# Kernel optimization log

Measured on AMD Instinct MI355X. Metric: run time of the kernel, lower is better.

The kernel has to match this reference:

```python
import jax, jax.numpy as jnp
import numpy as np

H, W, C = 64, 64, 2048
IMG = 224


def setup_inputs() -> dict:
    key = jax.random.key(0)
    features = jax.random.normal(key, (2, H, W, C), dtype=jnp.float32)
    return {"features": features, "img_size": IMG}


def reference(features, img_size):
    # features: [2, H, W, C] -- query (index 0) and target (index 1) feature maps.
    x0 = features[0]  # [H, W, C]
    x1 = features[1]  # [H, W, C]
    # Correlation volume: Decomposition[i,j,k,l] = sum_c x0[i,j,c] * x1[k,l,c]
    # (replaces the quadruple Python loop with a single GEMM-shaped einsum)
    decom = jnp.einsum('ijc,klc->ijkl', x0, x1)  # [H, W, H, W]
    decom = decom / jnp.max(decom)
    # NOTE: source calls `Decomposition.clamp(min=0)` without assignment -> no-op.
    decom_1 = jnp.sum(decom, axis=(2, 3))  # [H, W] saliency on query image
    decom_2 = jnp.sum(decom, axis=(0, 1))  # [H, W] saliency on target image
    stacked = jnp.stack((decom_1, decom_2))  # [2, H, W]
    # F.interpolate(mode='bilinear', align_corners=False) == half-pixel bilinear resize
    out = jax.image.resize(stacked, (2, img_size, img_size), method='bilinear')
    return out  # [2, img_size, img_size]
```

## Files before the change

kernel.cpp:

```cpp
#include <hip/hip_runtime.h>
#include <hip/hip_bf16.h>

#define HW    4096
#define CDIM  2048
#define IMG   224
#define NTKI  64
#define NTM   128
#define LROW  528
#define QSCALE 21.166666f

typedef int   int4v  __attribute__((ext_vector_type(4)));
typedef int   i32x16 __attribute__((ext_vector_type(16)));
typedef char  char4v __attribute__((ext_vector_type(4)));

__device__ __forceinline__ i32x16 zi16() {
    i32x16 z;
#pragma unroll
    for (int i = 0; i < 16; ++i) z[i] = 0;
    return z;
}
__device__ __forceinline__ char quant8(float x) {
    int r = __float2int_rn(x * QSCALE);
    r = min(max(r, -127), 127);
    return (char)r;
}

__global__ __launch_bounds__(256) void convert_pack_partial(
    const float* __restrict__ feat,
    char* __restrict__ Ap, char* __restrict__ Bp,
    float* __restrict__ P) {
    __shared__ char lds[64 * LROW];
    __shared__ float csum[512];
    const int tid = threadIdx.x;
    const int mat = blockIdx.z;
    const int rm  = blockIdx.y;
    const int kb0 = blockIdx.x * 512;
    const float* src = feat + (size_t)mat * HW * CDIM + (size_t)(rm * 64) * CDIM + kb0;

    const int cc = (tid & 127) * 4;
    float a0 = 0.f, a1 = 0.f, a2 = 0.f, a3 = 0.f;
#pragma unroll
    for (int j = 0; j < 32; ++j) {
        const int r = j * 2 + (tid >> 7);
        float4 v = *(const float4*)&src[(size_t)r * CDIM + cc];
        a0 += v.x; a1 += v.y; a2 += v.z; a3 += v.w;
        char4v q;
        q[0] = quant8(v.x); q[1] = quant8(v.y);
        q[2] = quant8(v.z); q[3] = quant8(v.w);
        *(char4v*)&lds[r * LROW + cc] = q;
    }
    if (tid >= 128) {
        csum[cc + 0] = a0; csum[cc + 1] = a1;
        csum[cc + 2] = a2; csum[cc + 3] = a3;
    }
    __syncthreads();
    if (tid < 128) {
        float4 p;
        p.x = a0 + csum[cc + 0]; p.y = a1 + csum[cc + 1];
        p.z = a2 + csum[cc + 2]; p.w = a3 + csum[cc + 3];
        *(float4*)&P[((size_t)mat * 64 + rm) * CDIM + kb0 + cc] = p;
    }

    const int l = tid & 63, w = tid >> 6;
    char* dstbase = mat ? Bp : Ap;
#pragma unroll
    for (int i = 0; i < 8; ++i) {
        const int t = w * 8 + i;
        const int tml = t >> 4, tkl = t & 15;
        int4v v = *(const int4v*)
            &lds[(tml * 32 + (l & 31)) * LROW + tkl * 32 + (l >> 5) * 16];
        const int tm  = rm * 2 + tml;
        const int tkg = blockIdx.x * 16 + tkl;
        *(int4v*)&dstbase[((size_t)(tm * NTKI + tkg) * 64 + l) * 16] = v;
    }
}

__global__ __launch_bounds__(256, 4) void gemm_max_kernel(
    const char* __restrict__ Ap, const char* __restrict__ Bp,
    const float* __restrict__ P, float* __restrict__ s,
    float* __restrict__ blockmax) {
    const int tid  = threadIdx.x;
    const int lane = tid & 63;
    const int wave = tid >> 6;
    const int wm = wave >> 1, wn = wave & 1;
    const int bm = blockIdx.y, bn = blockIdx.x;

    if (bm == 31 && bn < 16) {
        const int mat = bn >> 3;
        const int c = (bn & 7) * 256 + tid;
        const float* Pp = P + (size_t)mat * 64 * CDIM + c;
        float sum = 0.f;
#pragma unroll 8
        for (int r = 0; r < 64; ++r) sum += Pp[(size_t)r * CDIM];
        s[mat * CDIM + c] = sum;
    }

    const int tmA = bm * 4 + wm * 2;
    const int tnB = bn * 4 + wn * 2;
    const char* a0p = Ap + (size_t)(tmA * NTKI) * 1024 + lane * 16;
    const char* a1p = a0p + (size_t)NTKI * 1024;
    const char* b0p = Bp + (size_t)(tnB * NTKI) * 1024 + lane * 16;
    const char* b1p = b0p + (size_t)NTKI * 1024;

    i32x16 acc00 = zi16(), acc01 = zi16(), acc10 = zi16(), acc11 = zi16();

    int4v ca0 = *(const int4v*)a0p;
    int4v ca1 = *(const int4v*)a1p;
    int4v cb0 = *(const int4v*)b0p;
    int4v cb1 = *(const int4v*)b1p;

#pragma unroll 2
    for (int tk = 0; tk < NTKI - 1; ++tk) {
        const size_t o = (size_t)(tk + 1) * 1024;
        const int4v na0 = *(const int4v*)(a0p + o);
        const int4v na1 = *(const int4v*)(a1p + o);
        const int4v nb0 = *(const int4v*)(b0p + o);
        const int4v nb1 = *(const int4v*)(b1p + o);
        acc00 = __builtin_amdgcn_mfma_i32_32x32x32_i8(ca0, cb0, acc00, 0, 0, 0);
        acc01 = __builtin_amdgcn_mfma_i32_32x32x32_i8(ca0, cb1, acc01, 0, 0, 0);
        acc10 = __builtin_amdgcn_mfma_i32_32x32x32_i8(ca1, cb0, acc10, 0, 0, 0);
        acc11 = __builtin_amdgcn_mfma_i32_32x32x32_i8(ca1, cb1, acc11, 0, 0, 0);
        ca0 = na0; ca1 = na1; cb0 = nb0; cb1 = nb1;
    }
    acc00 = __builtin_amdgcn_mfma_i32_32x32x32_i8(ca0, cb0, acc00, 0, 0, 0);
    acc01 = __builtin_amdgcn_mfma_i32_32x32x32_i8(ca0, cb1, acc01, 0, 0, 0);
    acc10 = __builtin_amdgcn_mfma_i32_32x32x32_i8(ca1, cb0, acc10, 0, 0, 0);
    acc11 = __builtin_amdgcn_mfma_i32_32x32x32_i8(ca1, cb1, acc11, 0, 0, 0);

    int m = INT_MIN;
#pragma unroll
    for (int i = 0; i < 16; ++i) {
        m = max(m, acc00[i]); m = max(m, acc01[i]);
        m = max(m, acc10[i]); m = max(m, acc11[i]);
    }
#pragma unroll
    for (int off = 32; off; off >>= 1)
        m = max(m, __shfl_down(m, off));

    __shared__ int wred[4];
    if (lane == 0) wred[wave] = m;
    __syncthreads();
    if (tid == 0) {
        const int im = max(max(wred[0], wred[1]), max(wred[2], wred[3]));
        blockmax[blockIdx.y * gridDim.x + blockIdx.x] =
            (float)im * (1.0f / (QSCALE * QSCALE));
    }
}

__global__ __launch_bounds__(256) void saliency_kernel(
    const float* __restrict__ feat, const float* __restrict__ s,
    float* __restrict__ sal) {
    const int tid = threadIdx.x, lane = tid & 63, wave = tid >> 6;
    const int g = blockIdx.x * 4 + wave;
    const float* x;
    const float* sv;
    if (g < HW) { x = feat + (size_t)g * CDIM;                            sv = s + CDIM; }
    else        { x = feat + (size_t)HW * CDIM + (size_t)(g - HW) * CDIM; sv = s; }
    float acc = 0.f;
#pragma unroll
    for (int it = 0; it < 8; ++it) {
        const int c0 = it * 256 + lane * 4;
        float4 v = *(const float4*)&x[c0];
        float4 w = *(const float4*)&sv[c0];
        acc += v.x * w.x + v.y * w.y + v.z * w.z + v.w * w.w;
    }
#pragma unroll
    for (int off = 32; off; off >>= 1) acc += __shfl_down(acc, off);
    if (lane == 0) sal[g] = acc;
}

__global__ __launch_bounds__(256) void resize_kernel(
    const float* __restrict__ sal, const float* __restrict__ bmax,
    float* __restrict__ out) {
    __shared__ float w[4];
    __shared__ float rM;
    const int tid = threadIdx.x;
    float m = -3.4e38f;
    for (int i = tid; i < 1024; i += 256) m = fmaxf(m, bmax[i]);
#pragma unroll
    for (int off = 32; off; off >>= 1) m = fmaxf(m, __shfl_down(m, off));
    if ((tid & 63) == 0) w[tid >> 6] = m;
    __syncthreads();
    if (tid == 0)
        rM = 1.0f / fmaxf(fmaxf(w[0], w[1]), fmaxf(w[2], w[3]));
    __syncthreads();

    const int idx = blockIdx.x * 256 + tid;
    if (idx >= 2 * IMG * IMG) return;
    const int ch = idx / (IMG * IMG);
    const int rem = idx % (IMG * IMG);
    const int oy = rem / IMG, ox = rem % IMG;
    const float scale = 64.0f / (float)IMG;
    const float sy = ((float)oy + 0.5f) * scale - 0.5f;
    const float sx = ((float)ox + 0.5f) * scale - 0.5f;
    const float fy0 = floorf(sy), fx0 = floorf(sx);
    const float wy = sy - fy0, wx = sx - fx0;
    int y0 = (int)fy0, x0 = (int)fx0;
    int y1 = min(max(y0 + 1, 0), 63), x1 = min(max(x0 + 1, 0), 63);
    y0 = min(max(y0, 0), 63); x0 = min(max(x0, 0), 63);
    const float* p = sal + ch * HW;
    const float v00 = p[y0 * 64 + x0], v01 = p[y0 * 64 + x1];
    const float v10 = p[y1 * 64 + x0], v11 = p[y1 * 64 + x1];
    out[idx] = ((1.f - wy) * ((1.f - wx) * v00 + wx * v01) +
                wy * ((1.f - wx) * v10 + wx * v11)) * rM;
}

extern "C" void kernel_launch(void* const* d_in, const int* in_sizes, int n_in,
                              void* d_out, int out_size, void* d_ws, size_t ws_size,
                              hipStream_t stream) {
    const float* feat = (const float*)d_in[0];
    float* out = (float*)d_out;

    char* ws = (char*)d_ws;
    char* Ap = ws;
    char* Bp = ws + (size_t)8 * 1024 * 1024;
    float* P    = (float*)(ws + (size_t)16 * 1024 * 1024);
    float* s    = P + 2 * 64 * CDIM;
    float* bmax = s + 2 * CDIM;
    float* sal  = bmax + 1024;

    convert_pack_partial<<<dim3(4, 64, 2), 256, 0, stream>>>(feat, Ap, Bp, P);
    gemm_max_kernel<<<dim3(32, 32), 256, 0, stream>>>(Ap, Bp, P, s, bmax);
    saliency_kernel<<<2048, 256, 0, stream>>>(feat, s, sal);
    const int nout = 2 * IMG * IMG;
    resize_kernel<<<(nout + 255) / 256, 256, 0, stream>>>(sal, bmax, out);
}
```

Measured before the change: 147.7 us.

## Stage int8 GEMM tiles through LDS with async global_load_lds multi-buffering

The max-finding int8 GEMM now uses 256x256 block tiles with 8 waves. A/B fragments are streamed into a 4-deep LDS ring via global_load_lds, with explicit vmcnt waits and barriers, and MFMA runs at raised priority. Operands are now shared across waves instead of each wave reading its own fragments straight from global memory. The block count drops to 256 and the resize kernel's block-max reduction shrinks to match. The trade-off is 128KB of LDS per block, which limits occupancy, and fewer blocks than CUs.

```diff
diff --git a/kernel.cpp b/kernel.cpp
--- a/kernel.cpp
+++ b/kernel.cpp
@@ -8,6 +8,7 @@
 #define NTM   128
 #define LROW  528
 #define QSCALE 21.166666f
+#define NS    32
 
 typedef int   int4v  __attribute__((ext_vector_type(4)));
 typedef int   i32x16 __attribute__((ext_vector_type(16)));
@@ -23,6 +24,12 @@
     int r = __float2int_rn(x * QSCALE);
     r = min(max(r, -127), 127);
     return (char)r;
+}
+
+__device__ __forceinline__ void gload_lds16(const char* g, char* l) {
+    __builtin_amdgcn_global_load_lds(
+        (const __attribute__((address_space(1))) void*)g,
+        (__attribute__((address_space(3))) void*)l, 16, 0, 0);
 }
 
 __global__ __launch_bounds__(256) void convert_pack_partial(
@@ -75,73 +82,114 @@
     }
 }
 
-__global__ __launch_bounds__(256, 4) void gemm_max_kernel(
+__global__ __launch_bounds__(512, 2) void gemm_max_kernel(
     const char* __restrict__ Ap, const char* __restrict__ Bp,
     const float* __restrict__ P, float* __restrict__ s,
     float* __restrict__ blockmax) {
+    __shared__ char lds[4 * 32768];
+    __shared__ int wred[8];
     const int tid  = threadIdx.x;
     const int lane = tid & 63;
     const int wave = tid >> 6;
-    const int wm = wave >> 1, wn = wave & 1;
+    const int wm = wave >> 2, wn = wave & 3;
     const int bm = blockIdx.y, bn = blockIdx.x;
 
-    if (bm == 31 && bn < 16) {
-        const int mat = bn >> 3;
-        const int c = (bn & 7) * 256 + tid;
-        const float* Pp = P + (size_t)mat * 64 * CDIM + c;
+    const char* gb[4];
+    int loff[4];
+#pragma unroll
+    for (int q = 0; q < 4; ++q) {
+        const int c = wave * 4 + q;
+        const int kk = c & 1;
+        if (c < 16) {
+            const int il = c >> 1;
+            gb[q] = Ap + ((size_t)(bm * 8 + il) * NTKI + kk) * 1024 + lane * 16;
+            loff[q] = (il * 2 + kk) * 1024;
+        } else {
+            const int jl = (c - 16) >> 1;
+            gb[q] = Bp + ((size_t)(bn * 8 + jl) * NTKI + kk) * 1024 + lane * 16;
+            loff[q] = 16384 + (jl * 2 + kk) * 1024;
+        }
+    }
+
+#define ISSUE_STAGE(S) do {                                         \
+        char* buf_ = lds + (((S) & 3) << 15);                       \
+        _Pragma("unroll")                                           \
+        for (int q = 0; q < 4; ++q)                                 \
+            gload_lds16(gb[q] + (size_t)(S) * 2048, buf_ + loff[q]);\
+    } while (0)
+
+    ISSUE_STAGE(0); ISSUE_STAGE(1); ISSUE_STAGE(2);
+
+    if (bm == 0 && bn < 16 && tid < 256) {
+        const int gc = bn * 256 + tid;
+        const float* Pp = P + (size_t)(gc >> 11) * 64 * CDIM + (gc & 2047);
         float sum = 0.f;
 #pragma unroll 8
         for (int r = 0; r < 64; ++r) sum += Pp[(size_t)r * CDIM];
-        s[mat * CDIM + c] = sum;
-    }
-
-    const int tmA = bm * 4 + wm * 2;
-    const int tnB = bn * 4 + wn * 2;
-    const char* a0p = Ap + (size_t)(tmA * NTKI) * 1024 + lane * 16;
-    const char* a1p = a0p + (size_t)NTKI * 1024;
-    const char* b0p = Bp + (size_t)(tnB * NTKI) * 1024 + lane * 16;
-    const char* b1p = b0p + (size_t)NTKI * 1024;
-
-    i32x16 acc00 = zi16(), acc01 = zi16(), acc10 = zi16(), acc11 = zi16();
-
-    int4v ca0 = *(const int4v*)a0p;
-    int4v ca1 = *(const int4v*)a1p;
-    int4v cb0 = *(const int4v*)b0p;
-    int4v cb1 = *(const int4v*)b1p;
-
-#pragma unroll 2
-    for (int tk = 0; tk < NTKI - 1; ++tk) {
-        const size_t o = (size_t)(tk + 1) * 1024;
-        const int4v na0 = *(const int4v*)(a0p + o);
-        const int4v na1 = *(const int4v*)(a1p + o);
-        const int4v nb0 = *(const int4v*)(b0p + o);
-        const int4v nb1 = *(const int4v*)(b1p + o);
-        acc00 = __builtin_amdgcn_mfma_i32_32x32x32_i8(ca0, cb0, acc00, 0, 0, 0);
-        acc01 = __builtin_amdgcn_mfma_i32_32x32x32_i8(ca0, cb1, acc01, 0, 0, 0);
-        acc10 = __builtin_amdgcn_mfma_i32_32x32x32_i8(ca1, cb0, acc10, 0, 0, 0);
-        acc11 = __builtin_amdgcn_mfma_i32_32x32x32_i8(ca1, cb1, acc11, 0, 0, 0);
-        ca0 = na0; ca1 = na1; cb0 = nb0; cb1 = nb1;
-    }
-    acc00 = __builtin_amdgcn_mfma_i32_32x32x32_i8(ca0, cb0, acc00, 0, 0, 0);
-    acc01 = __builtin_amdgcn_mfma_i32_32x32x32_i8(ca0, cb1, acc01, 0, 0, 0);
-    acc10 = __builtin_amdgcn_mfma_i32_32x32x32_i8(ca1, cb0, acc10, 0, 0, 0);
-    acc11 = __builtin_amdgcn_mfma_i32_32x32x32_i8(ca1, cb1, acc11, 0, 0, 0);
+        s[gc] = sum;
+    }
+
+    asm volatile("s_waitcnt vmcnt(8)" ::: "memory");
+    asm volatile("s_barrier" ::: "memory");
+
+    const int abase = wm * 8192 + lane * 16;
+    const int bbase = 16384 + wn * 4096 + lane * 16;
+
+    i32x16 acc00 = zi16(), acc01 = zi16();
+    i32x16 acc10 = zi16(), acc11 = zi16();
+    i32x16 acc20 = zi16(), acc21 = zi16();
+    i32x16 acc30 = zi16(), acc31 = zi16();
+
+    for (int st = 0; st < NS; ++st) {
+        if (st + 3 < NS) ISSUE_STAGE(st + 3);
+
+        const char* base = lds + ((st & 3) << 15);
+#pragma unroll
+        for (int kk = 0; kk < 2; ++kk) {
+            const char* ab = base + abase + kk * 1024;
+            const char* bb = base + bbase + kk * 1024;
+            int4v a0 = *(const int4v*)(ab);
+            int4v a1 = *(const int4v*)(ab + 2048);
+            int4v a2 = *(const int4v*)(ab + 4096);
+            int4v a3 = *(const int4v*)(ab + 6144);
+            int4v b0 = *(const int4v*)(bb);
+            int4v b1 = *(const int4v*)(bb + 2048);
+            __builtin_amdgcn_s_setprio(1);
+            acc00 = __builtin_amdgcn_mfma_i32_32x32x32_i8(a0, b0, acc00, 0, 0, 0);
+            acc01 = __builtin_amdgcn_mfma_i32_32x32x32_i8(a0, b1, acc01, 0, 0, 0);
+            acc10 = __builtin_amdgcn_mfma_i32_32x32x32_i8(a1, b0, acc10, 0, 0, 0);
+            acc11 = __builtin_amdgcn_mfma_i32_32x32x32_i8(a1, b1, acc11, 0, 0, 0);
+            acc20 = __builtin_amdgcn_mfma_i32_32x32x32_i8(a2, b0, acc20, 0, 0, 0);
+            acc21 = __builtin_amdgcn_mfma_i32_32x32x32_i8(a2, b1, acc21, 0, 0, 0);
+            acc30 = __builtin_amdgcn_mfma_i32_32x32x32_i8(a3, b0, acc30, 0, 0, 0);
+            acc31 = __builtin_amdgcn_mfma_i32_32x32x32_i8(a3, b1, acc31, 0, 0, 0);
+            __builtin_amdgcn_s_setprio(0);
+        }
+
+        if (st < NS - 3)      { asm volatile("s_waitcnt vmcnt(8)" ::: "memory"); }
+        else if (st == NS - 3){ asm volatile("s_waitcnt vmcnt(4)" ::: "memory"); }
+        else if (st == NS - 2){ asm volatile("s_waitcnt vmcnt(0)" ::: "memory"); }
+        if (st < NS - 1) asm volatile("s_barrier" ::: "memory");
+    }
+#undef ISSUE_STAGE
 
     int m = INT_MIN;
 #pragma unroll
     for (int i = 0; i < 16; ++i) {
         m = max(m, acc00[i]); m = max(m, acc01[i]);
         m = max(m, acc10[i]); m = max(m, acc11[i]);
+        m = max(m, acc20[i]); m = max(m, acc21[i]);
+        m = max(m, acc30[i]); m = max(m, acc31[i]);
     }
 #pragma unroll
     for (int off = 32; off; off >>= 1)
         m = max(m, __shfl_down(m, off));
-
-    __shared__ int wred[4];
     if (lane == 0) wred[wave] = m;
     __syncthreads();
     if (tid == 0) {
-        const int im = max(max(wred[0], wred[1]), max(wred[2], wred[3]));
+        int im = wred[0];
+#pragma unroll
+        for (int w2 = 1; w2 < 8; ++w2) im = max(im, wred[w2]);
         blockmax[blockIdx.y * gridDim.x + blockIdx.x] =
             (float)im * (1.0f / (QSCALE * QSCALE));
     }
@@ -176,7 +224,7 @@
     __shared__ float rM;
     const int tid = threadIdx.x;
     float m = -3.4e38f;
-    for (int i = tid; i < 1024; i += 256) m = fmaxf(m, bmax[i]);
+    for (int i = tid; i < 256; i += 256) m = fmaxf(m, bmax[i]);
 #pragma unroll
     for (int off = 32; off; off >>= 1) m = fmaxf(m, __shfl_down(m, off));
     if ((tid & 63) == 0) w[tid >> 6] = m;
@@ -220,7 +268,7 @@
     float* sal  = bmax + 1024;
 
     convert_pack_partial<<<dim3(4, 64, 2), 256, 0, stream>>>(feat, Ap, Bp, P);
-    gemm_max_kernel<<<dim3(32, 32), 256, 0, stream>>>(Ap, Bp, P, s, bmax);
+    gemm_max_kernel<<<dim3(16, 16), 512, 0, stream>>>(Ap, Bp, P, s, bmax);
     saliency_kernel<<<2048, 256, 0, stream>>>(feat, s, sal);
     const int nout = 2 * IMG * IMG;
     resize_kernel<<<(nout + 255) / 256, 256, 0, stream>>>(sal, bmax, out);
```

After: 144.9 us. About the same (-1.9%).

## Enlarge GEMM-max tiles to 256x256 with LDS-staged B and XCD-aware block mapping

Applied to the files above, without the earlier changes.

The int8 GEMM-max kernel moves from 128x128 tiles with 4 waves to 256x256 tiles with 8 waves. Each wave now holds a 4x2 grid of 32x32 accumulators, and B tiles are streamed into a triple-buffered LDS ring with direct global-to-LDS loads. A is register double-buffered, MFMA issue gets raised priority, and blocks are remapped so neighbouring tiles share an XCD for L2 reuse. The aim is to cut redundant global traffic for A and B operands. The cost is higher register pressure and hand-tuned vmcnt waits that must match the number of loads in flight.

```diff
diff --git a/kernel.cpp b/kernel.cpp
--- a/kernel.cpp
+++ b/kernel.cpp
@@ -8,6 +8,8 @@
 #define NTM   128
 #define LROW  528
 #define QSCALE 21.166666f
+#define NS    32
+#define BSB   16384
 
 typedef int   int4v  __attribute__((ext_vector_type(4)));
 typedef int   i32x16 __attribute__((ext_vector_type(16)));
@@ -23,6 +25,12 @@
     int r = __float2int_rn(x * QSCALE);
     r = min(max(r, -127), 127);
     return (char)r;
+}
+
+__device__ __forceinline__ void gload_lds16(const char* g, char* l) {
+    __builtin_amdgcn_global_load_lds(
+        (const __attribute__((address_space(1))) void*)g,
+        (__attribute__((address_space(3))) void*)l, 16, 0, 0);
 }
 
 __global__ __launch_bounds__(256) void convert_pack_partial(
@@ -75,75 +83,125 @@
     }
 }
 
-__global__ __launch_bounds__(256, 4) void gemm_max_kernel(
+__global__ __launch_bounds__(512, 2) void gemm_max_kernel(
     const char* __restrict__ Ap, const char* __restrict__ Bp,
     const float* __restrict__ P, float* __restrict__ s,
     float* __restrict__ blockmax) {
+    __shared__ char lds[3 * BSB];
+    __shared__ int wred[8];
     const int tid  = threadIdx.x;
     const int lane = tid & 63;
     const int wave = tid >> 6;
-    const int wm = wave >> 1, wn = wave & 1;
-    const int bm = blockIdx.y, bn = blockIdx.x;
-
-    if (bm == 31 && bn < 16) {
-        const int mat = bn >> 3;
-        const int c = (bn & 7) * 256 + tid;
-        const float* Pp = P + (size_t)mat * 64 * CDIM + c;
+    const int wm = wave >> 2, wn = wave & 3;
+
+    const int bid = blockIdx.y * gridDim.x + blockIdx.x;
+    const int xcd = bid & 7;
+    const int wix = bid >> 3;
+    const int bm  = (xcd >> 2) * 8 + (wix >> 2);
+    const int bn  = (xcd & 3) * 4 + (wix & 3);
+
+    const char* gB0 = Bp + (size_t)(bn * 8 + wave) * NTKI * 1024 + lane * 16;
+    const char* gB1 = gB0 + 1024;
+    const int lo0 = wave * 2048;
+    const int lo1 = lo0 + 1024;
+
+#define ISSUE_B(S, BUF) do {                                   \
+        gload_lds16(gB0 + (size_t)(S) * 2048, (BUF) + lo0);    \
+        gload_lds16(gB1 + (size_t)(S) * 2048, (BUF) + lo1);    \
+    } while (0)
+
+    const char* ga[4];
+#pragma unroll
+    for (int i = 0; i < 4; ++i)
+        ga[i] = Ap + (size_t)(bm * 8 + wm * 4 + i) * NTKI * 1024 + lane * 16;
+
+#define LOAD_A(SET, S) do {                                               \
+        _Pragma("unroll")                                                 \
+        for (int i = 0; i < 4; ++i) {                                     \
+            SET[i][0] = *(const int4v*)(ga[i] + (size_t)(S) * 2048);      \
+            SET[i][1] = *(const int4v*)(ga[i] + (size_t)(S) * 2048 + 1024); \
+        }                                                                 \
+    } while (0)
+
+    char* r0 = lds;
+    char* r1 = lds + BSB;
+    char* r2 = lds + 2 * BSB;
+
+    int4v xa[4][2], ya[4][2];
+
+    ISSUE_B(0, r0); ISSUE_B(1, r1);
+    LOAD_A(xa, 0);
+
+    if (bm == 15 && tid < 256) {
+        const int gc = bn * 256 + tid;
+        const float* Pp = P + (size_t)(gc >> 11) * 64 * CDIM + (gc & 2047);
         float sum = 0.f;
 #pragma unroll 8
         for (int r = 0; r < 64; ++r) sum += Pp[(size_t)r * CDIM];
-        s[mat * CDIM + c] = sum;
-    }
-
-    const int tmA = bm * 4 + wm * 2;
-    const int tnB = bn * 4 + wn * 2;
-    const char* a0p = Ap + (size_t)(tmA * NTKI) * 1024 + lane * 16;
-    const char* a1p = a0p + (size_t)NTKI * 1024;
-    const char* b0p = Bp + (size_t)(tnB * NTKI) * 1024 + lane * 16;
-    const char* b1p = b0p + (size_t)NTKI * 1024;
-
-    i32x16 acc00 = zi16(), acc01 = zi16(), acc10 = zi16(), acc11 = zi16();
-
-    int4v ca0 = *(const int4v*)a0p;
-    int4v ca1 = *(const int4v*)a1p;
-    int4v cb0 = *(const int4v*)b0p;
-    int4v cb1 = *(const int4v*)b1p;
-
-#pragma unroll 2
-    for (int tk = 0; tk < NTKI - 1; ++tk) {
-        const size_t o = (size_t)(tk + 1) * 1024;
-        const int4v na0 = *(const int4v*)(a0p + o);
-        const int4v na1 = *(const int4v*)(a1p + o);
-        const int4v nb0 = *(const int4v*)(b0p + o);
-        const int4v nb1 = *(const int4v*)(b1p + o);
-        acc00 = __builtin_amdgcn_mfma_i32_32x32x32_i8(ca0, cb0, acc00, 0, 0, 0);
-        acc01 = __builtin_amdgcn_mfma_i32_32x32x32_i8(ca0, cb1, acc01, 0, 0, 0);
-        acc10 = __builtin_amdgcn_mfma_i32_32x32x32_i8(ca1, cb0, acc10, 0, 0, 0);
-        acc11 = __builtin_amdgcn_mfma_i32_32x32x32_i8(ca1, cb1, acc11, 0, 0, 0);
-        ca0 = na0; ca1 = na1; cb0 = nb0; cb1 = nb1;
-    }
-    acc00 = __builtin_amdgcn_mfma_i32_32x32x32_i8(ca0, cb0, acc00, 0, 0, 0);
-    acc01 = __builtin_amdgcn_mfma_i32_32x32x32_i8(ca0, cb1, acc01, 0, 0, 0);
-    acc10 = __builtin_amdgcn_mfma_i32_32x32x32_i8(ca1, cb0, acc10, 0, 0, 0);
-    acc11 = __builtin_amdgcn_mfma_i32_32x32x32_i8(ca1, cb1, acc11, 0, 0, 0);
+        s[gc] = sum;
+    }
+
+    asm volatile("s_waitcnt vmcnt(10)" ::: "memory");
+    asm volatile("s_barrier" ::: "memory");
+
+    i32x16 acc[4][2];
+#pragma unroll
+    for (int i = 0; i < 4; ++i) {
+        acc[i][0] = zi16(); acc[i][1] = zi16();
+    }
+
+    const int bof = wn * 4096 + lane * 16;
+
+#define MM(i, j, A, B) acc[i][j] = __builtin_amdgcn_mfma_i32_32x32x32_i8(A, B, acc[i][j], 0, 0, 0)
+#define STAGE_BODY(CURA, NXTA, ST)                                          \
+    do {                                                                    \
+        if ((ST) + 2 < NS) ISSUE_B((ST) + 2, r2);                           \
+        if ((ST) + 1 < NS) LOAD_A(NXTA, (ST) + 1);                          \
+        int4v b00 = *(const int4v*)(r0 + bof);                \
+        int4v b01 = *(const int4v*)(r0 + bof + 1024);         \
+        int4v b10 = *(const int4v*)(r0 + bof + 2048);         \
+        int4v b11 = *(const int4v*)(r0 + bof + 3072);         \
+        __builtin_amdgcn_s_setprio(1);                                      \
+        _Pragma("unroll")                                                   \
+        for (int i = 0; i < 4; ++i) { MM(i,0,CURA[i][0],b00); MM(i,1,CURA[i][0],b10); } \
+        _Pragma("unroll")                                                   \
+        for (int i = 0; i < 4; ++i) { MM(i,0,CURA[i][1],b01); MM(i,1,CURA[i][1],b11); } \
+        __builtin_amdgcn_s_setprio(0);                                      \
+        if ((ST) < NS - 2)                                                  \
+            asm volatile("s_waitcnt vmcnt(10)" ::: "memory");               \
+        else if ((ST) == NS - 2)                                            \
+            asm volatile("s_waitcnt vmcnt(8)" ::: "memory");                \
+        if ((ST) < NS - 1) asm volatile("s_barrier" ::: "memory");          \
+        char* t_ = r0; r0 = r1; r1 = r2; r2 = t_;                           \
+    } while (0)
+
+    for (int it = 0; it < 16; ++it) {
+        STAGE_BODY(xa, ya, 2 * it);
+        STAGE_BODY(ya, xa, 2 * it + 1);
+    }
+#undef STAGE_BODY
+#undef MM
+#undef ISSUE_B
+#undef LOAD_A
 
     int m = INT_MIN;
 #pragma unroll
-    for (int i = 0; i < 16; ++i) {
-        m = max(m, acc00[i]); m = max(m, acc01[i]);
-        m = max(m, acc10[i]); m = max(m, acc11[i]);
-    }
+    for (int i = 0; i < 4; ++i)
+#pragma unroll
+        for (int j = 0; j < 2; ++j)
+#pragma unroll
+            for (int e = 0; e < 16; ++e)
+                m = max(m, acc[i][j][e]);
 #pragma unroll
     for (int off = 32; off; off >>= 1)
         m = max(m, __shfl_down(m, off));
-
-    __shared__ int wred[4];
     if (lane == 0) wred[wave] = m;
     __syncthreads();
     if (tid == 0) {
-        const int im = max(max(wred[0], wred[1]), max(wred[2], wred[3]));
-        blockmax[blockIdx.y * gridDim.x + blockIdx.x] =
-            (float)im * (1.0f / (QSCALE * QSCALE));
+        int im = wred[0];
+#pragma unroll
+        for (int w2 = 1; w2 < 8; ++w2) im = max(im, wred[w2]);
+        blockmax[bid] = (float)im * (1.0f / (QSCALE * QSCALE));
     }
 }
 
@@ -176,7 +234,7 @@
     __shared__ float rM;
     const int tid = threadIdx.x;
     float m = -3.4e38f;
-    for (int i = tid; i < 1024; i += 256) m = fmaxf(m, bmax[i]);
+    for (int i = tid; i < 256; i += 256) m = fmaxf(m, bmax[i]);
 #pragma unroll
     for (int off = 32; off; off >>= 1) m = fmaxf(m, __shfl_down(m, off));
     if ((tid & 63) == 0) w[tid >> 6] = m;
@@ -220,7 +278,7 @@
     float* sal  = bmax + 1024;
 
     convert_pack_partial<<<dim3(4, 64, 2), 256, 0, stream>>>(feat, Ap, Bp, P);
-    gemm_max_kernel<<<dim3(32, 32), 256, 0, stream>>>(Ap, Bp, P, s, bmax);
+    gemm_max_kernel<<<dim3(16, 16), 512, 0, stream>>>(Ap, Bp, P, s, bmax);
     saliency_kernel<<<2048, 256, 0, stream>>>(feat, s, sal);
     const int nout = 2 * IMG * IMG;
     resize_kernel<<<(nout + 255) / 256, 256, 0, stream>>>(sal, bmax, out);
```

After: 145.2 us. Within noise of the previous version (-1.6%).
